# Performance work log

Hardware: AMD Instinct MI355X
Metric: run time of the kernel (lower is better)

Reference implementation:

```python
import jax, jax.numpy as jnp
import numpy as np

NEG_INF = -9e15  # matches the torch -9000000000000000.0 mask value
LRELU_SLOPE = 0.01  # torch nn.LeakyReLU default


def setup_inputs() -> dict:
    key = jax.random.key(0)
    k1, k2, k3, k4 = jax.random.split(key, 4)
    N, F_in, F_out = 8192, 256, 128
    x = jax.random.normal(k1, (N, F_in), dtype=jnp.float32)
    adj = jax.random.randint(k2, (N, N), 0, 2, dtype=jnp.int32)
    # xavier_uniform with gain=1.414
    limW = 1.414 * np.sqrt(6.0 / (F_in + F_out))
    W = jax.random.uniform(k3, (F_in, F_out), minval=-limW, maxval=limW, dtype=jnp.float32)
    lima = 1.414 * np.sqrt(6.0 / (2 * F_out + 1))
    a = jax.random.uniform(k4, (2 * F_out, 1), minval=-lima, maxval=lima, dtype=jnp.float32)
    return {"x": x, "adj": adj, "W": W, "a": a}


def reference(x, adj, W, a):
    # h: [N, F_out]
    h = x @ W
    F_out = h.shape[1]
    a1 = a[:F_out, 0]   # attention vector for source node i
    a2 = a[F_out:, 0]   # attention vector for target node j
    # e[i, j] = leaky_relu(h_i . a1 + h_j . a2) -- equivalent to the repeat/cat
    # construction without materializing the [N, N, 2F] tensor.
    e = (h @ a1)[:, None] + (h @ a2)[None, :]  # [N, N]
    e = jnp.where(e > 0, e, LRELU_SLOPE * e)
    scores = jnp.where(adj > 0, e, NEG_INF)
    attention = jax.nn.softmax(scores, axis=1)  # dropout omitted (eval mode)
    h_prime = attention @ h  # [N, F_out]
    return jax.nn.elu(h_prime)
```

## Files before the change

### kernel.cpp

```cpp
#include <hip/hip_runtime.h>
#include <hip/hip_bf16.h>
#include <stdint.h>


#define N_NODES 8192
#define F_INF   256
#define F_OUT   128
#define LRELU   0.01f

typedef __bf16 bf16x8 __attribute__((ext_vector_type(8)));
typedef float  f32x4  __attribute__((ext_vector_type(4)));
using bf16 = __hip_bfloat16;

__device__ __forceinline__ float b2f(bf16 v) { return __bfloat162float(v); }
__device__ __forceinline__ bf16  f2b(float v) { return __float2bfloat16(v); }

__global__ __launch_bounds__(256) void k_xw(const float* __restrict__ x,
                                            const float* __restrict__ W,
                                            const float* __restrict__ a,
                                            bf16* __restrict__ hT,
                                            float* __restrict__ s1,
                                            float* __restrict__ s2) {
    __shared__ __align__(16) bf16 WT[F_OUT][F_INF + 8];
    __shared__ __align__(16) bf16 XS[64][72];
    __shared__ float waL[2 * F_INF];
    __shared__ float s1L[64], s2L[64];
    const int tid  = threadIdx.x;
    const int lane = tid & 63, wave = tid >> 6;
    const int i0   = blockIdx.x * 64;
    waL[tid] = 0.f; waL[F_INF + tid] = 0.f;
    if (tid < 64) { s1L[tid] = 0.f; s2L[tid] = 0.f; }
    __syncthreads();
    for (int idx = tid; idx < (F_INF * F_OUT) / 8; idx += 256) {
        int k  = idx >> 4;
        int n0 = (idx & 15) * 8;
        const float* src = W + (size_t)k * F_OUT + n0;
        float4 va = *(const float4*)(src);
        float4 vb = *(const float4*)(src + 4);
        float v[8] = {va.x, va.y, va.z, va.w, vb.x, vb.y, vb.z, vb.w};
        float p1 = 0.f, p2 = 0.f;
#pragma unroll
        for (int c = 0; c < 8; ++c) {
            WT[n0 + c][k] = f2b(v[c]);
            p1 += v[c] * a[n0 + c];
            p2 += v[c] * a[F_OUT + n0 + c];
        }
        atomicAdd(&waL[k], p1);
        atomicAdd(&waL[F_INF + k], p2);
    }
    __syncthreads();
    f32x4 acc[8];
#pragma unroll
    for (int t = 0; t < 8; ++t) acc[t] = {0.f, 0.f, 0.f, 0.f};
    const int m = lane & 15, quad = lane >> 4;
    const int rt = wave;
    for (int kc = 0; kc < F_INF / 64; ++kc) {
        const int k0 = kc * 64;
        {
            int part = tid & 7;
            int r    = tid >> 3;
#pragma unroll
            for (int p = 0; p < 2; ++p) {
                int rr = r + p * 32;
                const float* src = x + (size_t)(i0 + rr) * F_INF + k0 + part * 8;
                float4 va = *(const float4*)(src);
                float4 vb = *(const float4*)(src + 4);
                float v[8] = {va.x, va.y, va.z, va.w, vb.x, vb.y, vb.z, vb.w};
                __align__(16) bf16 th[8];
                float q1 = 0.f, q2 = 0.f;
#pragma unroll
                for (int c = 0; c < 8; ++c) {
                    th[c] = f2b(v[c]);
                    q1 += v[c] * waL[k0 + part * 8 + c];
                    q2 += v[c] * waL[F_INF + k0 + part * 8 + c];
                }
                *(uint4*)(&XS[rr][part * 8]) = *(const uint4*)th;
                atomicAdd(&s1L[rr], q1);
                atomicAdd(&s2L[rr], q2);
            }
        }
        __syncthreads();
#pragma unroll
        for (int ks = 0; ks < 2; ++ks) {
            bf16x8 af = *(const bf16x8*)(&XS[rt * 16 + m][ks * 32 + quad * 8]);
#pragma unroll
            for (int ct = 0; ct < 8; ++ct) {
                bf16x8 bfr = *(const bf16x8*)(&WT[ct * 16 + m][kc * 64 + ks * 32 + quad * 8]);
                acc[ct] = __builtin_amdgcn_mfma_f32_16x16x32_bf16(af, bfr, acc[ct], 0, 0, 0);
            }
        }
        __syncthreads();
    }
#pragma unroll
    for (int ct = 0; ct < 8; ++ct) {
        const int f = ct * 16 + m;
#pragma unroll
        for (int r = 0; r < 4; ++r) {
            const int i = i0 + rt * 16 + quad * 4 + r;
            hT[(size_t)f * N_NODES + i] = f2b(acc[ct][r]);
        }
    }
    if (tid < 64) { s1[i0 + tid] = s1L[tid]; s2[i0 + tid] = s2L[tid]; }
}

__global__ __launch_bounds__(256) void k_max(const float* __restrict__ s2,
                                             float* __restrict__ mg) {
    __shared__ float red[256];
    int tid = threadIdx.x;
    float m = -1e30f;
    for (int j = tid; j < N_NODES; j += 256) m = fmaxf(m, s2[j]);
    red[tid] = m;
    __syncthreads();
    for (int s = 128; s > 0; s >>= 1) {
        if (tid < s) red[tid] = fmaxf(red[tid], red[tid + s]);
        __syncthreads();
    }
    if (tid == 0) mg[0] = red[0];
}

__global__ __launch_bounds__(256) void k_attn(const int* __restrict__ adj,
                                              const float* __restrict__ s1g,
                                              const float* __restrict__ s2g,
                                              const float* __restrict__ mg,
                                              const bf16* __restrict__ hT,
                                              float* __restrict__ Of,
                                              float* __restrict__ lp) {
    __shared__ __align__(16) bf16 HS[2][F_OUT][72];
    __shared__ float s2s[1024];
    const int tid  = threadIdx.x;
    const int lane = tid & 63, wave = tid >> 6;
    const int m = lane & 15, quad = lane >> 4;
    const int i0    = blockIdx.x * 64;
    const int jq    = blockIdx.y;
    const int jbase = jq * 1024;
    const int irow  = i0 + wave * 16 + m;
    const float s1v = s1g[irow];
    const float tmi = s1v + mg[0];
    const float mi  = fmaxf(tmi, LRELU * tmi);
    *(float4*)&s2s[tid * 4] = *(const float4*)(s2g + jbase + tid * 4);
    const int part = tid & 7, fr = tid >> 3;
    const bf16* hTp = hT + jbase + part * 8;
    {
        uint4 v0 = *(const uint4*)(hTp + (size_t)(fr +  0) * N_NODES);
        uint4 v1 = *(const uint4*)(hTp + (size_t)(fr + 32) * N_NODES);
        uint4 v2 = *(const uint4*)(hTp + (size_t)(fr + 64) * N_NODES);
        uint4 v3 = *(const uint4*)(hTp + (size_t)(fr + 96) * N_NODES);
        *(uint4*)&HS[0][fr +  0][part * 8] = v0;
        *(uint4*)&HS[0][fr + 32][part * 8] = v1;
        *(uint4*)&HS[0][fr + 64][part * 8] = v2;
        *(uint4*)&HS[0][fr + 96][part * 8] = v3;
    }
    uint4 h0 = *(const uint4*)(hTp + (size_t)(fr +  0) * N_NODES + 64);
    uint4 h1 = *(const uint4*)(hTp + (size_t)(fr + 32) * N_NODES + 64);
    uint4 h2 = *(const uint4*)(hTp + (size_t)(fr + 64) * N_NODES + 64);
    uint4 h3 = *(const uint4*)(hTp + (size_t)(fr + 96) * N_NODES + 64);
    const int4* arowp = (const int4*)(adj + (size_t)irow * N_NODES + jbase);
    int4 avA[4], avB[4];
    avA[0] = arowp[quad * 2];          avA[1] = arowp[quad * 2 + 1];
    avA[2] = arowp[8 + quad * 2];      avA[3] = arowp[8 + quad * 2 + 1];
    avB[0] = arowp[16 + quad * 2];     avB[1] = arowp[16 + quad * 2 + 1];
    avB[2] = arowp[16 + 8 + quad * 2]; avB[3] = arowp[16 + 8 + quad * 2 + 1];
    float lacc = 0.f;
    f32x4 acc[8];
#pragma unroll
    for (int c = 0; c < 8; ++c) acc[c] = {0.f, 0.f, 0.f, 0.f};
    __syncthreads();
    int b = 0;

    for (int jc = 0; jc < 16; ++jc) {
        if (jc < 15) {
            *(uint4*)&HS[b ^ 1][fr +  0][part * 8] = h0;
            *(uint4*)&HS[b ^ 1][fr + 32][part * 8] = h1;
            *(uint4*)&HS[b ^ 1][fr + 64][part * 8] = h2;
            *(uint4*)&HS[b ^ 1][fr + 96][part * 8] = h3;
        }
        bf16x8 afrag[2];
#pragma unroll
        for (int kh = 0; kh < 2; ++kh) {
            const int am[8] = {avA[kh*2].x, avA[kh*2].y, avA[kh*2].z, avA[kh*2].w,
                               avA[kh*2+1].x, avA[kh*2+1].y, avA[kh*2+1].z, avA[kh*2+1].w};
            const float* s2p = &s2s[jc * 64 + kh * 32 + quad * 8];
            __align__(16) bf16 a8[8];
#pragma unroll
            for (int t = 0; t < 8; ++t) {
                float e = s1v + s2p[t];
                e = fmaxf(e, LRELU * e);
                float w = (am[t] > 0) ? __expf(e - mi) : 0.f;
                bf16 bb = f2b(w);
                a8[t] = bb;
                lacc += b2f(bb);
            }
            afrag[kh] = *(const bf16x8*)a8;
        }
#pragma unroll
        for (int q = 0; q < 4; ++q) avA[q] = avB[q];
        if (jc < 14) {
            const int base = (jc + 2) * 16;
            avB[0] = arowp[base + quad * 2];     avB[1] = arowp[base + quad * 2 + 1];
            avB[2] = arowp[base + 8 + quad * 2]; avB[3] = arowp[base + 8 + quad * 2 + 1];
        }
        if (jc < 14) {
            const int off = (jc + 2) * 64;
            h0 = *(const uint4*)(hTp + (size_t)(fr +  0) * N_NODES + off);
            h1 = *(const uint4*)(hTp + (size_t)(fr + 32) * N_NODES + off);
            h2 = *(const uint4*)(hTp + (size_t)(fr + 64) * N_NODES + off);
            h3 = *(const uint4*)(hTp + (size_t)(fr + 96) * N_NODES + off);
        }
#pragma unroll
        for (int kh = 0; kh < 2; ++kh)
#pragma unroll
            for (int c = 0; c < 8; ++c) {
                bf16x8 bfr = *(const bf16x8*)(&HS[b][c * 16 + m][kh * 32 + quad * 8]);
                acc[c] = __builtin_amdgcn_mfma_f32_16x16x32_bf16(afrag[kh], bfr, acc[c], 0, 0, 0);
            }
        __syncthreads();
        b ^= 1;
    }
    lacc += __shfl_xor(lacc, 16);
    lacc += __shfl_xor(lacc, 32);
    if (quad == 0) lp[(size_t)jq * N_NODES + irow] = lacc;
#pragma unroll
    for (int c = 0; c < 8; ++c) {
        const int f = c * 16 + m;
#pragma unroll
        for (int r = 0; r < 4; ++r) {
            const int i = i0 + wave * 16 + quad * 4 + r;
            Of[((size_t)jq * N_NODES + i) * F_OUT + f] = acc[c][r];
        }
    }
}

__global__ __launch_bounds__(256) void k_comb(const float* __restrict__ Of,
                                              const float* __restrict__ lp,
                                              float* __restrict__ out) {
    size_t gid = (size_t)blockIdx.x * 256 + threadIdx.x;
    int i = (int)(gid >> 7);
    float s = 0.f, l = 0.f;
#pragma unroll
    for (int q = 0; q < 8; ++q) {
        s += Of[(size_t)q * (N_NODES * (size_t)F_OUT) + gid];
        l += lp[q * N_NODES + i];
    }
    float o = s / l;
    out[gid] = o > 0.f ? o : __expf(o) - 1.f;
}

extern "C" void kernel_launch(void* const* d_in, const int* in_sizes, int n_in,
                              void* d_out, int out_size, void* d_ws, size_t ws_size,
                              hipStream_t stream) {
    (void)out_size; (void)ws_size;
    const float* x   = nullptr;
    const int*   adj = nullptr;
    const float* W   = nullptr;
    const float* a   = nullptr;
    for (int ii = 0; ii < n_in; ++ii) {
        int sz = in_sizes[ii];
        if      (sz == N_NODES * F_INF)  x   = (const float*)d_in[ii];
        else if (sz == F_INF * F_OUT)    W   = (const float*)d_in[ii];
        else if (sz == 2 * F_OUT)        a   = (const float*)d_in[ii];
        else                             adj = (const int*)d_in[ii];
    }
    float* out = (float*)d_out;

    char* ws = (char*)d_ws;
    bf16*  hT = (bf16*)ws;  ws += (size_t)F_OUT * N_NODES * 2;
    float* s1 = (float*)ws; ws += N_NODES * 4;
    float* s2 = (float*)ws; ws += N_NODES * 4;
    float* mg = (float*)ws; ws += 256;
    float* lp = (float*)ws; ws += 8 * N_NODES * 4;
    float* Of = (float*)ws;

    k_xw  <<<N_NODES / 64, 256, 0, stream>>>(x, W, a, hT, s1, s2);
    k_max <<<1, 256, 0, stream>>>(s2, mg);
    k_attn<<<dim3(N_NODES / 64, 8), 256, 0, stream>>>(adj, s1, s2, mg, hT, Of, lp);
    k_comb<<<(N_NODES * F_OUT) / 256, 256, 0, stream>>>(Of, lp, out);
}
```

Baseline: 467.7 us.

## Load hT MFMA B-fragments directly from global into registers, drop LDS staging

Removes the double-buffered shared-memory tile of hT and the per-iteration __syncthreads. Each lane now loads its MFMA B-operand fragments directly from global memory into registers, split into two half-sets (hA/hB) that are prefetched in an interleaved way around the MFMA groups. This is meant to cut LDS write/read traffic and barrier stalls. In exchange, every wave in the block reloads the same hT data from global/L2 (4x redundant reads), register pressure rises, and there is less latency hiding for the hB loads issued in the same iteration.

```diff
diff --git a/kernel.cpp b/kernel.cpp
--- a/kernel.cpp
+++ b/kernel.cpp
@@ -125,7 +125,6 @@
                                               const bf16* __restrict__ hT,
                                               float* __restrict__ Of,
                                               float* __restrict__ lp) {
-    __shared__ __align__(16) bf16 HS[2][F_OUT][72];
     __shared__ float s2s[1024];
     const int tid  = threadIdx.x;
     const int lane = tid & 63, wave = tid >> 6;
@@ -138,48 +137,38 @@
     const float tmi = s1v + mg[0];
     const float mi  = fmaxf(tmi, LRELU * tmi);
     *(float4*)&s2s[tid * 4] = *(const float4*)(s2g + jbase + tid * 4);
-    const int part = tid & 7, fr = tid >> 3;
-    const bf16* hTp = hT + jbase + part * 8;
-    {
-        uint4 v0 = *(const uint4*)(hTp + (size_t)(fr +  0) * N_NODES);
-        uint4 v1 = *(const uint4*)(hTp + (size_t)(fr + 32) * N_NODES);
-        uint4 v2 = *(const uint4*)(hTp + (size_t)(fr + 64) * N_NODES);
-        uint4 v3 = *(const uint4*)(hTp + (size_t)(fr + 96) * N_NODES);
-        *(uint4*)&HS[0][fr +  0][part * 8] = v0;
-        *(uint4*)&HS[0][fr + 32][part * 8] = v1;
-        *(uint4*)&HS[0][fr + 64][part * 8] = v2;
-        *(uint4*)&HS[0][fr + 96][part * 8] = v3;
-    }
-    uint4 h0 = *(const uint4*)(hTp + (size_t)(fr +  0) * N_NODES + 64);
-    uint4 h1 = *(const uint4*)(hTp + (size_t)(fr + 32) * N_NODES + 64);
-    uint4 h2 = *(const uint4*)(hTp + (size_t)(fr + 64) * N_NODES + 64);
-    uint4 h3 = *(const uint4*)(hTp + (size_t)(fr + 96) * N_NODES + 64);
+    const bf16* hlane = hT + (size_t)m * N_NODES + jbase + quad * 8;
     const int4* arowp = (const int4*)(adj + (size_t)irow * N_NODES + jbase);
     int4 avA[4], avB[4];
     avA[0] = arowp[quad * 2];          avA[1] = arowp[quad * 2 + 1];
     avA[2] = arowp[8 + quad * 2];      avA[3] = arowp[8 + quad * 2 + 1];
     avB[0] = arowp[16 + quad * 2];     avB[1] = arowp[16 + quad * 2 + 1];
     avB[2] = arowp[16 + 8 + quad * 2]; avB[3] = arowp[16 + 8 + quad * 2 + 1];
+    uint4 hA[8], hB[8];
+#pragma unroll
+    for (int c = 0; c < 4; ++c)
+#pragma unroll
+        for (int kh = 0; kh < 2; ++kh)
+            hA[c * 2 + kh] = *(const uint4*)(hlane + (size_t)(c * 16) * N_NODES + kh * 32);
     float lacc = 0.f;
     f32x4 acc[8];
 #pragma unroll
     for (int c = 0; c < 8; ++c) acc[c] = {0.f, 0.f, 0.f, 0.f};
     __syncthreads();
-    int b = 0;
 
     for (int jc = 0; jc < 16; ++jc) {
-        if (jc < 15) {
-            *(uint4*)&HS[b ^ 1][fr +  0][part * 8] = h0;
-            *(uint4*)&HS[b ^ 1][fr + 32][part * 8] = h1;
-            *(uint4*)&HS[b ^ 1][fr + 64][part * 8] = h2;
-            *(uint4*)&HS[b ^ 1][fr + 96][part * 8] = h3;
-        }
+        const int jo = jc * 64;
+#pragma unroll
+        for (int c = 0; c < 4; ++c)
+#pragma unroll
+            for (int kh = 0; kh < 2; ++kh)
+                hB[c * 2 + kh] = *(const uint4*)(hlane + (size_t)((c + 4) * 16) * N_NODES + jo + kh * 32);
         bf16x8 afrag[2];
 #pragma unroll
         for (int kh = 0; kh < 2; ++kh) {
             const int am[8] = {avA[kh*2].x, avA[kh*2].y, avA[kh*2].z, avA[kh*2].w,
                                avA[kh*2+1].x, avA[kh*2+1].y, avA[kh*2+1].z, avA[kh*2+1].w};
-            const float* s2p = &s2s[jc * 64 + kh * 32 + quad * 8];
+            const float* s2p = &s2s[jo + kh * 32 + quad * 8];
             __align__(16) bf16 a8[8];
 #pragma unroll
             for (int t = 0; t < 8; ++t) {
@@ -199,22 +188,25 @@
             avB[0] = arowp[base + quad * 2];     avB[1] = arowp[base + quad * 2 + 1];
             avB[2] = arowp[base + 8 + quad * 2]; avB[3] = arowp[base + 8 + quad * 2 + 1];
         }
-        if (jc < 14) {
-            const int off = (jc + 2) * 64;
-            h0 = *(const uint4*)(hTp + (size_t)(fr +  0) * N_NODES + off);
-            h1 = *(const uint4*)(hTp + (size_t)(fr + 32) * N_NODES + off);
-            h2 = *(const uint4*)(hTp + (size_t)(fr + 64) * N_NODES + off);
-            h3 = *(const uint4*)(hTp + (size_t)(fr + 96) * N_NODES + off);
-        }
 #pragma unroll
         for (int kh = 0; kh < 2; ++kh)
 #pragma unroll
-            for (int c = 0; c < 8; ++c) {
-                bf16x8 bfr = *(const bf16x8*)(&HS[b][c * 16 + m][kh * 32 + quad * 8]);
-                acc[c] = __builtin_amdgcn_mfma_f32_16x16x32_bf16(afrag[kh], bfr, acc[c], 0, 0, 0);
-            }
-        __syncthreads();
-        b ^= 1;
+            for (int c = 0; c < 4; ++c)
+                acc[c] = __builtin_amdgcn_mfma_f32_16x16x32_bf16(
+                    afrag[kh], *(const bf16x8*)&hA[c * 2 + kh], acc[c], 0, 0, 0);
+        if (jc < 15) {
+#pragma unroll
+            for (int c = 0; c < 4; ++c)
+#pragma unroll
+                for (int kh = 0; kh < 2; ++kh)
+                    hA[c * 2 + kh] = *(const uint4*)(hlane + (size_t)(c * 16) * N_NODES + jo + 64 + kh * 32);
+        }
+#pragma unroll
+        for (int kh = 0; kh < 2; ++kh)
+#pragma unroll
+            for (int c = 0; c < 4; ++c)
+                acc[c + 4] = __builtin_amdgcn_mfma_f32_16x16x32_bf16(
+                    afrag[kh], *(const bf16x8*)&hB[c * 2 + kh], acc[c + 4], 0, 0, 0);
     }
     lacc += __shfl_xor(lacc, 16);
     lacc += __shfl_xor(lacc, 32);
```

After: 499.6 us. +6.8%, slower.
